# Optimization experiments

Measured on AMD Instinct MI355X. Metric: run time of the kernel, lower is better.

Reference implementation:

```python
import jax, jax.numpy as jnp
import numpy as np

HIDDEN = 4096
RANK = 4
DELTA = 1.0
BATCH = 4096


def glorot(key, shape):
    return jax.random.uniform(key, shape, minval=-1.0, maxval=1.0) * jnp.sqrt(2.0 / sum(shape))


def setup_inputs() -> dict:
    key = jax.random.key(0)
    k1, k2, k3, k4, k5, k6 = jax.random.split(key, 6)
    return {
        "h": jax.random.normal(k5, (BATCH, HIDDEN), dtype=jnp.float32),
        "x": jax.random.normal(k6, (BATCH, HIDDEN), dtype=jnp.float32),
        "a_diag": glorot(k1, (HIDDEN,)),
        "p_vec": glorot(k2, (HIDDEN, RANK)),
        "q_vec": glorot(k3, (HIDDEN, RANK)),
        "b_mat": glorot(k4, (HIDDEN, HIDDEN)),
    }


def reference(h, x, a_diag, p_vec, q_vec, b_mat):
    # Per-sample original math: (I + delta*(diag(a) + p q^T)) @ h + delta * b_mat.T @ x
    # Batched (rows of h/x are samples) with the Woodbury-style low-rank form:
    #   A_disc @ h  ->  h + delta*(a*h + (h @ q) @ p^T)
    #   B_disc^T @ x -> delta * (x @ b_mat)
    Ah = h + DELTA * (h * a_diag + (h @ q_vec) @ p_vec.T)  # [B, N]
    Bx = DELTA * (x @ b_mat)                               # [B, N]
    return Ah + Bx
```

## Files before the change

kernel.cpp:

```cpp
#include <hip/hip_runtime.h>
#include <hip/hip_bf16.h>
#include <stdint.h>
#include <stddef.h>

#define HIDDEN 4096
#define BATCH  4096
#define RANK   4

typedef _Float16 f16;
typedef __attribute__((ext_vector_type(8))) _Float16 half8;
typedef __attribute__((ext_vector_type(4))) float f32x4;
typedef __attribute__((ext_vector_type(8))) unsigned short ushort8;

#define ASYNC_COPY16(g, l)                                                     \
  __builtin_amdgcn_global_load_lds(                                            \
      (__attribute__((address_space(1))) void*)(g),                            \
      (__attribute__((address_space(3))) void*)(l), 16, 0, 0)

__global__ void cast_f16_kernel(const float* __restrict__ src, f16* __restrict__ dst) {
  size_t i = ((size_t)blockIdx.x * blockDim.x + threadIdx.x) * 8;
  float4 v0 = *(const float4*)(src + i);
  float4 v1 = *(const float4*)(src + i + 4);
  union { f16 h[8]; ushort8 v; } u;
  u.h[0] = (f16)v0.x; u.h[1] = (f16)v0.y; u.h[2] = (f16)v0.z; u.h[3] = (f16)v0.w;
  u.h[4] = (f16)v1.x; u.h[5] = (f16)v1.y; u.h[6] = (f16)v1.z; u.h[7] = (f16)v1.w;
  *(ushort8*)(dst + i) = u.v;
}

__global__ void transpose_cast_kernel(const float* __restrict__ B, f16* __restrict__ Bt) {
  __shared__ __align__(16) f16 tile[64 * 64];
  const int t = threadIdx.x;
  const int bx = blockIdx.x;
  const int by = blockIdx.y;
  const int tx = t & 15, ty = t >> 4;
  #pragma unroll
  for (int i = 0; i < 4; i++) {
    const int k = ty + i * 16;
    float4 v = *(const float4*)(B + (size_t)(by * 64 + k) * HIDDEN + bx * 64 + tx * 4);
    f16 hv[4];
    hv[0] = (f16)v.x; hv[1] = (f16)v.y; hv[2] = (f16)v.z; hv[3] = (f16)v.w;
    #pragma unroll
    for (int c = 0; c < 4; c++) {
      const int n = tx * 4 + c;
      const int phys = (k >> 3) ^ ((n >> 2) & 7);
      tile[n * 64 + phys * 8 + (k & 7)] = hv[c];
    }
  }
  __syncthreads();
  const int wx = t & 7, wy = t >> 3;
  #pragma unroll
  for (int i = 0; i < 2; i++) {
    const int n = wy + i * 32;
    const int phys = wx ^ ((n >> 2) & 7);
    ushort8 v = *(ushort8*)&tile[n * 64 + phys * 8];
    *(ushort8*)(Bt + (size_t)(bx * 64 + n) * HIDDEN + by * 64 + wx * 8) = v;
  }
}

__global__ void hq_kernel(const float* __restrict__ h, const float* __restrict__ q,
                          float* __restrict__ hq) {
  const int b = blockIdx.x;
  const float* hrow = h + (size_t)b * HIDDEN;
  float a0 = 0.f, a1 = 0.f, a2 = 0.f, a3 = 0.f;
  for (int k = threadIdx.x; k < HIDDEN; k += 256) {
    float hv = hrow[k];
    float4 qv = *(const float4*)(q + (size_t)k * RANK);
    a0 += hv * qv.x; a1 += hv * qv.y; a2 += hv * qv.z; a3 += hv * qv.w;
  }
  #pragma unroll
  for (int off = 32; off; off >>= 1) {
    a0 += __shfl_down(a0, off, 64);
    a1 += __shfl_down(a1, off, 64);
    a2 += __shfl_down(a2, off, 64);
    a3 += __shfl_down(a3, off, 64);
  }
  __shared__ float red[4][4];
  const int wave = threadIdx.x >> 6, lane = threadIdx.x & 63;
  if (lane == 0) { red[wave][0] = a0; red[wave][1] = a1; red[wave][2] = a2; red[wave][3] = a3; }
  __syncthreads();
  if (threadIdx.x < 4) {
    float s = red[0][threadIdx.x] + red[1][threadIdx.x] + red[2][threadIdx.x] + red[3][threadIdx.x];
    hq[(size_t)b * RANK + threadIdx.x] = s;
  }
}

#define GBM 256
#define GBN 256
#define GBK 64

#define BARRIER()                                   \
  do {                                              \
    asm volatile("" ::: "memory");                  \
    __builtin_amdgcn_s_barrier();                   \
    asm volatile("" ::: "memory");                  \
  } while (0)

#define VMWAIT0() asm volatile("s_waitcnt vmcnt(0)" ::: "memory")

#define STAGE_TILE(SBUF)                                                     \
  do {                                                                       \
    char* ad_ = (char*)(&As[SBUF][0]) + wave * 1024;                         \
    char* bd_ = (char*)(&Bs[SBUF][0]) + wave * 1024;                         \
    ASYNC_COPY16(ag + (size_t)0 * 64 * HIDDEN, ad_ + 0 * 8192);              \
    ASYNC_COPY16(bg + (size_t)0 * 64 * HIDDEN, bd_ + 0 * 8192);              \
    ASYNC_COPY16(ag + (size_t)1 * 64 * HIDDEN, ad_ + 1 * 8192);              \
    ASYNC_COPY16(bg + (size_t)1 * 64 * HIDDEN, bd_ + 1 * 8192);              \
    ASYNC_COPY16(ag + (size_t)2 * 64 * HIDDEN, ad_ + 2 * 8192);              \
    ASYNC_COPY16(bg + (size_t)2 * 64 * HIDDEN, bd_ + 2 * 8192);              \
    ASYNC_COPY16(ag + (size_t)3 * 64 * HIDDEN, ad_ + 3 * 8192);              \
    ASYNC_COPY16(bg + (size_t)3 * 64 * HIDDEN, bd_ + 3 * 8192);              \
    ag += GBK; bg += GBK;                                                    \
  } while (0)

#define LDF(base, R16, SG) (*(const half8*)((base) + (R16) * (16 * GBK) + (SG)))

#define MFMA4(I, AF)                                                                    \
  acc[I][0] = __builtin_amdgcn_mfma_f32_16x16x32_f16(AF, bf0, acc[I][0], 0, 0, 0);      \
  acc[I][1] = __builtin_amdgcn_mfma_f32_16x16x32_f16(AF, bf1, acc[I][1], 0, 0, 0);      \
  acc[I][2] = __builtin_amdgcn_mfma_f32_16x16x32_f16(AF, bf2, acc[I][2], 0, 0, 0);      \
  acc[I][3] = __builtin_amdgcn_mfma_f32_16x16x32_f16(AF, bf3, acc[I][3], 0, 0, 0);

#define TILE(BUF, SBUF, DO_STAGE)                                            \
  {                                                                          \
    const f16* Ab_ = &As[BUF][0] + (wm * 128 + fm) * GBK;                    \
    const f16* Bb_ = &Bs[BUF][0] + (wn * 64 + fm) * GBK;                     \
    const int sg0_ = ((0 + q) ^ sw) * 8;                                     \
    const int sg1_ = ((4 + q) ^ sw) * 8;                                     \
    half8 a0, a1, a2, a3, bf0, bf1, bf2, bf3;                                \
                         \
    a0 = LDF(Ab_, 0, sg0_); a1 = LDF(Ab_, 1, sg0_);                          \
    a2 = LDF(Ab_, 2, sg0_); a3 = LDF(Ab_, 3, sg0_);                          \
    bf0 = LDF(Bb_, 0, sg0_); bf1 = LDF(Bb_, 1, sg0_);                        \
    bf2 = LDF(Bb_, 2, sg0_); bf3 = LDF(Bb_, 3, sg0_);                        \
    if (DO_STAGE) STAGE_TILE(SBUF);                                          \
    BARRIER();                                                               \
    __builtin_amdgcn_s_setprio(1);                                           \
    MFMA4(0, a0) MFMA4(1, a1) MFMA4(2, a2) MFMA4(3, a3)                      \
    __builtin_amdgcn_s_setprio(0);                                           \
    BARRIER();                                                               \
                              \
    a0 = LDF(Ab_, 4, sg0_); a1 = LDF(Ab_, 5, sg0_);                          \
    a2 = LDF(Ab_, 6, sg0_); a3 = LDF(Ab_, 7, sg0_);                          \
    BARRIER();                                                               \
    __builtin_amdgcn_s_setprio(1);                                           \
    MFMA4(4, a0) MFMA4(5, a1) MFMA4(6, a2) MFMA4(7, a3)                      \
    __builtin_amdgcn_s_setprio(0);                                           \
    BARRIER();                                                               \
                                            \
    a0 = LDF(Ab_, 0, sg1_); a1 = LDF(Ab_, 1, sg1_);                          \
    a2 = LDF(Ab_, 2, sg1_); a3 = LDF(Ab_, 3, sg1_);                          \
    bf0 = LDF(Bb_, 0, sg1_); bf1 = LDF(Bb_, 1, sg1_);                        \
    bf2 = LDF(Bb_, 2, sg1_); bf3 = LDF(Bb_, 3, sg1_);                        \
    BARRIER();                                                               \
    __builtin_amdgcn_s_setprio(1);                                           \
    MFMA4(0, a0) MFMA4(1, a1) MFMA4(2, a2) MFMA4(3, a3)                      \
    __builtin_amdgcn_s_setprio(0);                                           \
    BARRIER();                                                               \
         \
    a0 = LDF(Ab_, 4, sg1_); a1 = LDF(Ab_, 5, sg1_);                          \
    a2 = LDF(Ab_, 6, sg1_); a3 = LDF(Ab_, 7, sg1_);                          \
    BARRIER();                                                               \
    __builtin_amdgcn_s_setprio(1);                                           \
    MFMA4(4, a0) MFMA4(5, a1) MFMA4(6, a2) MFMA4(7, a3)                      \
    __builtin_amdgcn_s_setprio(0);                                           \
    VMWAIT0();                                                               \
    BARRIER();                                                               \
  }

__global__ __launch_bounds__(512, 2) void gemm_fused_kernel(
    const f16* __restrict__ Xb, const f16* __restrict__ Bt,
    const float* __restrict__ h, const float* __restrict__ a_diag,
    const float* __restrict__ p_vec, const float* __restrict__ hq,
    float* __restrict__ out) {
  __shared__ __align__(16) f16 As[2][GBM * GBK];
  __shared__ __align__(16) f16 Bs[2][GBN * GBK];
  const int tid = threadIdx.x;
  const int bm = blockIdx.x, bn = blockIdx.y;
  const int wave = tid >> 6, lane = tid & 63;
  const int wm = wave >> 2, wn = wave & 3;

  const int srow = tid >> 3;
  const int gseg = (tid & 7) ^ (srow & 7);
  const f16* ag = Xb + (size_t)(bm * GBM + srow) * HIDDEN + gseg * 8;
  const f16* bg = Bt + (size_t)(bn * GBN + srow) * HIDDEN + gseg * 8;

  f32x4 acc[8][4];
  #pragma unroll
  for (int i = 0; i < 8; i++)
    #pragma unroll
    for (int j = 0; j < 4; j++)
      acc[i][j] = (f32x4){0.f, 0.f, 0.f, 0.f};

  const int q = lane >> 4;
  const int fm = lane & 15;
  const int sw = fm & 7;

  STAGE_TILE(0);
  VMWAIT0();
  BARRIER();

  #pragma unroll 1
  for (int kt2 = 0; kt2 < 31; ++kt2) {
    TILE(0, 1, true)
    TILE(1, 0, true)
  }
  TILE(0, 1, true)
  TILE(1, 0, false)

  float ad[4];
  float4 pv[4];
  #pragma unroll
  for (int j = 0; j < 4; j++) {
    const int gn = bn * GBN + wn * 64 + j * 16 + fm;
    ad[j] = 1.0f + a_diag[gn];
    pv[j] = *(const float4*)(p_vec + (size_t)gn * RANK);
  }
  #pragma unroll
  for (int i = 0; i < 8; i++) {
    #pragma unroll
    for (int r = 0; r < 4; r++) {
      const size_t gb = (size_t)(bm * GBM + wm * 128 + i * 16 + q * 4 + r);
      const float4 hv = *(const float4*)(hq + gb * RANK);
      const size_t rowoff = gb * HIDDEN + bn * GBN + wn * 64 + fm;
      #pragma unroll
      for (int j = 0; j < 4; j++) {
        const size_t idx = rowoff + j * 16;
        const float hval = __builtin_nontemporal_load(&h[idx]);
        const float v = acc[i][j][r] + hval * ad[j] +
                        hv.x * pv[j].x + hv.y * pv[j].y + hv.z * pv[j].z + hv.w * pv[j].w;
        __builtin_nontemporal_store(v, &out[idx]);
      }
    }
  }
}

__global__ void gemm_f32_fallback_kernel(const float* __restrict__ x, const float* __restrict__ bmat,
                                         const float* __restrict__ h, const float* __restrict__ a_diag,
                                         const float* __restrict__ p_vec, const float* __restrict__ hq,
                                         float* __restrict__ out) {
  __shared__ float As[16][64];
  __shared__ float Bs[16][68];
  const int t = threadIdx.x;
  const int bx = blockIdx.x, by = blockIdx.y;
  const int tm = t & 15, tn = t >> 4;
  float acc[4][4] = {{0.f}};
  for (int k0 = 0; k0 < HIDDEN; k0 += 16) {
    #pragma unroll
    for (int l = 0; l < 4; l++) {
      int idx = t + l * 256;
      int r = idx >> 4, k = idx & 15;
      As[k][r] = x[(size_t)(by * 64 + r) * HIDDEN + k0 + k];
      int kb = idx >> 6, nb = idx & 63;
      Bs[kb][nb] = bmat[(size_t)(k0 + kb) * HIDDEN + bx * 64 + nb];
    }
    __syncthreads();
    #pragma unroll
    for (int k = 0; k < 16; k++) {
      float av[4], bv[4];
      #pragma unroll
      for (int ii = 0; ii < 4; ii++) av[ii] = As[k][tm * 4 + ii];
      #pragma unroll
      for (int jj = 0; jj < 4; jj++) bv[jj] = Bs[k][tn * 4 + jj];
      #pragma unroll
      for (int ii = 0; ii < 4; ii++)
        #pragma unroll
        for (int jj = 0; jj < 4; jj++)
          acc[ii][jj] += av[ii] * bv[jj];
    }
    __syncthreads();
  }
  #pragma unroll
  for (int jj = 0; jj < 4; jj++) {
    int gn = bx * 64 + tn * 4 + jj;
    float ad = 1.0f + a_diag[gn];
    float4 pv = *(const float4*)(p_vec + (size_t)gn * RANK);
    #pragma unroll
    for (int ii = 0; ii < 4; ii++) {
      size_t gb = (size_t)(by * 64 + tm * 4 + ii);
      float4 hv = *(const float4*)(hq + gb * RANK);
      size_t idx = gb * HIDDEN + gn;
      out[idx] = acc[ii][jj] + h[idx] * ad +
                 hv.x * pv.x + hv.y * pv.y + hv.z * pv.z + hv.w * pv.w;
    }
  }
}

extern "C" void kernel_launch(void* const* d_in, const int* in_sizes, int n_in,
                              void* d_out, int out_size, void* d_ws, size_t ws_size,
                              hipStream_t stream) {
  const float* h      = (const float*)d_in[0];
  const float* x      = (const float*)d_in[1];
  const float* a_diag = (const float*)d_in[2];
  const float* p_vec  = (const float*)d_in[3];
  const float* q_vec  = (const float*)d_in[4];
  const float* b_mat  = (const float*)d_in[5];
  float* out = (float*)d_out;

  const size_t nElem = (size_t)BATCH * HIDDEN;
  const size_t hq_bytes = (size_t)BATCH * RANK * sizeof(float);
  const size_t need = hq_bytes + 2 * nElem * sizeof(f16);

  float* hq = (float*)d_ws;
  hq_kernel<<<BATCH, 256, 0, stream>>>(h, q_vec, hq);

  if (ws_size >= need) {
    f16* Xb = (f16*)((char*)d_ws + hq_bytes);
    f16* Bt = Xb + nElem;
    cast_f16_kernel<<<nElem / 2048, 256, 0, stream>>>(x, Xb);
    transpose_cast_kernel<<<dim3(HIDDEN / 64, HIDDEN / 64), 256, 0, stream>>>(b_mat, Bt);
    gemm_fused_kernel<<<dim3(BATCH / GBM, HIDDEN / GBN), 512, 0, stream>>>(
        Xb, Bt, h, a_diag, p_vec, hq, out);
  } else {
    gemm_f32_fallback_kernel<<<dim3(HIDDEN / 64, BATCH / 64), 256, 0, stream>>>(
        x, b_mat, h, a_diag, p_vec, hq, out);
  }
}
```

Before: 370.3 us.

## Spread global-to-LDS tile staging across compute phases with partial vmcnt waits

Each tile's eight async global-to-LDS copies are now split into four groups: B rows 0-1, B rows 2-3, A chunks 0/2 and A chunks 1/3. Each group is issued in a different MFMA phase instead of all at once. The end-of-tile wait changes from vmcnt(0) to vmcnt(2), so the last A-chunk copies can still be in flight when the next tile starts. The first phase of that tile only reads A chunks 0/2, and a mid-tile vmcnt(2) ensures chunks 1/3 have landed before they are read. The aim is to spread memory issue across the loop and shorten the full drain at each tile boundary, at the cost of tighter wait-count reasoning that must stay exactly in sync with the issue order.

```diff
diff --git a/kernel.cpp b/kernel.cpp
--- a/kernel.cpp
+++ b/kernel.cpp
@@ -96,19 +96,32 @@
   } while (0)
 
 #define VMWAIT0() asm volatile("s_waitcnt vmcnt(0)" ::: "memory")
-
-#define STAGE_TILE(SBUF)                                                     \
+#define VMWAIT2() asm volatile("s_waitcnt vmcnt(2)" ::: "memory")
+#define VMNOP()   do { } while (0)
+
+#define STAGE_B01(SBUF)                                                      \
+  do {                                                                       \
+    char* bd_ = (char*)(&Bs[SBUF][0]) + wave * 1024;                         \
+    ASYNC_COPY16(bg + (size_t)0 * 64 * HIDDEN, bd_ + 0 * 8192);              \
+    ASYNC_COPY16(bg + (size_t)1 * 64 * HIDDEN, bd_ + 1 * 8192);              \
+  } while (0)
+#define STAGE_B23(SBUF)                                                      \
+  do {                                                                       \
+    char* bd_ = (char*)(&Bs[SBUF][0]) + wave * 1024;                         \
+    ASYNC_COPY16(bg + (size_t)2 * 64 * HIDDEN, bd_ + 2 * 8192);              \
+    ASYNC_COPY16(bg + (size_t)3 * 64 * HIDDEN, bd_ + 3 * 8192);              \
+  } while (0)
+#define STAGE_A02(SBUF)                                                      \
   do {                                                                       \
     char* ad_ = (char*)(&As[SBUF][0]) + wave * 1024;                         \
-    char* bd_ = (char*)(&Bs[SBUF][0]) + wave * 1024;                         \
     ASYNC_COPY16(ag + (size_t)0 * 64 * HIDDEN, ad_ + 0 * 8192);              \
-    ASYNC_COPY16(bg + (size_t)0 * 64 * HIDDEN, bd_ + 0 * 8192);              \
+    ASYNC_COPY16(ag + (size_t)2 * 64 * HIDDEN, ad_ + 2 * 8192);              \
+  } while (0)
+#define STAGE_A13(SBUF)                                                      \
+  do {                                                                       \
+    char* ad_ = (char*)(&As[SBUF][0]) + wave * 1024;                         \
     ASYNC_COPY16(ag + (size_t)1 * 64 * HIDDEN, ad_ + 1 * 8192);              \
-    ASYNC_COPY16(bg + (size_t)1 * 64 * HIDDEN, bd_ + 1 * 8192);              \
-    ASYNC_COPY16(ag + (size_t)2 * 64 * HIDDEN, ad_ + 2 * 8192);              \
-    ASYNC_COPY16(bg + (size_t)2 * 64 * HIDDEN, bd_ + 2 * 8192);              \
     ASYNC_COPY16(ag + (size_t)3 * 64 * HIDDEN, ad_ + 3 * 8192);              \
-    ASYNC_COPY16(bg + (size_t)3 * 64 * HIDDEN, bd_ + 3 * 8192);              \
     ag += GBK; bg += GBK;                                                    \
   } while (0)
 
@@ -120,27 +133,29 @@
   acc[I][2] = __builtin_amdgcn_mfma_f32_16x16x32_f16(AF, bf2, acc[I][2], 0, 0, 0);      \
   acc[I][3] = __builtin_amdgcn_mfma_f32_16x16x32_f16(AF, bf3, acc[I][3], 0, 0, 0);
 
-#define TILE(BUF, SBUF, DO_STAGE)                                            \
+#define TILE(BUF, SBUF, DO_STAGE, WAITP0, WAITEND)                           \
   {                                                                          \
     const f16* Ab_ = &As[BUF][0] + (wm * 128 + fm) * GBK;                    \
     const f16* Bb_ = &Bs[BUF][0] + (wn * 64 + fm) * GBK;                     \
     const int sg0_ = ((0 + q) ^ sw) * 8;                                     \
     const int sg1_ = ((4 + q) ^ sw) * 8;                                     \
     half8 a0, a1, a2, a3, bf0, bf1, bf2, bf3;                                \
-                         \
+                                            \
     a0 = LDF(Ab_, 0, sg0_); a1 = LDF(Ab_, 1, sg0_);                          \
     a2 = LDF(Ab_, 2, sg0_); a3 = LDF(Ab_, 3, sg0_);                          \
     bf0 = LDF(Bb_, 0, sg0_); bf1 = LDF(Bb_, 1, sg0_);                        \
     bf2 = LDF(Bb_, 2, sg0_); bf3 = LDF(Bb_, 3, sg0_);                        \
-    if (DO_STAGE) STAGE_TILE(SBUF);                                          \
+    if (DO_STAGE) STAGE_B01(SBUF);                                           \
     BARRIER();                                                               \
     __builtin_amdgcn_s_setprio(1);                                           \
     MFMA4(0, a0) MFMA4(1, a1) MFMA4(2, a2) MFMA4(3, a3)                      \
     __builtin_amdgcn_s_setprio(0);                                           \
-    BARRIER();                                                               \
-                              \
+    WAITP0;                                                                  \
+    BARRIER();                                                               \
+                   \
     a0 = LDF(Ab_, 4, sg0_); a1 = LDF(Ab_, 5, sg0_);                          \
     a2 = LDF(Ab_, 6, sg0_); a3 = LDF(Ab_, 7, sg0_);                          \
+    if (DO_STAGE) STAGE_B23(SBUF);                                           \
     BARRIER();                                                               \
     __builtin_amdgcn_s_setprio(1);                                           \
     MFMA4(4, a0) MFMA4(5, a1) MFMA4(6, a2) MFMA4(7, a3)                      \
@@ -151,19 +166,21 @@
     a2 = LDF(Ab_, 2, sg1_); a3 = LDF(Ab_, 3, sg1_);                          \
     bf0 = LDF(Bb_, 0, sg1_); bf1 = LDF(Bb_, 1, sg1_);                        \
     bf2 = LDF(Bb_, 2, sg1_); bf3 = LDF(Bb_, 3, sg1_);                        \
+    if (DO_STAGE) STAGE_A02(SBUF);                                           \
     BARRIER();                                                               \
     __builtin_amdgcn_s_setprio(1);                                           \
     MFMA4(0, a0) MFMA4(1, a1) MFMA4(2, a2) MFMA4(3, a3)                      \
     __builtin_amdgcn_s_setprio(0);                                           \
     BARRIER();                                                               \
-         \
+                                            \
     a0 = LDF(Ab_, 4, sg1_); a1 = LDF(Ab_, 5, sg1_);                          \
     a2 = LDF(Ab_, 6, sg1_); a3 = LDF(Ab_, 7, sg1_);                          \
+    if (DO_STAGE) STAGE_A13(SBUF);                                           \
     BARRIER();                                                               \
     __builtin_amdgcn_s_setprio(1);                                           \
     MFMA4(4, a0) MFMA4(5, a1) MFMA4(6, a2) MFMA4(7, a3)                      \
     __builtin_amdgcn_s_setprio(0);                                           \
-    VMWAIT0();                                                               \
+    WAITEND;                                                                 \
     BARRIER();                                                               \
   }
 
@@ -195,17 +212,17 @@
   const int fm = lane & 15;
   const int sw = fm & 7;
 
-  STAGE_TILE(0);
-  VMWAIT0();
+  STAGE_B01(0); STAGE_B23(0); STAGE_A02(0); STAGE_A13(0);
+  VMWAIT2();
   BARRIER();
 
   #pragma unroll 1
   for (int kt2 = 0; kt2 < 31; ++kt2) {
-    TILE(0, 1, true)
-    TILE(1, 0, true)
-  }
-  TILE(0, 1, true)
-  TILE(1, 0, false)
+    TILE(0, 1, 1, VMWAIT2(), VMWAIT2())
+    TILE(1, 0, 1, VMWAIT2(), VMWAIT2())
+  }
+  TILE(0, 1, 1, VMWAIT2(), VMWAIT2())
+  TILE(1, 0, 0, VMWAIT0(), VMNOP())
 
   float ad[4];
   float4 pv[4];
```

Measured after the change: 362.1 us. 2.2% less time.

## Collapse per-tile barriers and overlap LDS fragment loads with MFMA; remap block indices

Applied to the files above, without the earlier changes.

Restructures the GEMM inner tile so there is one barrier per K-tile instead of about eight. It double-registers the A and B fragments (aA/aB, bE/bO) so LDS reads for the next MFMA quad are issued while the current quad runs, with sched_barrier fences to keep that order. It also remaps the linear block index so each group of blocks with the same index mod 8 (likely landing on one XCD) shares a compact set of bm/bn tiles, which should improve L2 reuse. This raises register pressure and relies on the single barrier plus the trailing vmcnt wait to keep the double-buffered LDS correct.

```diff
diff --git a/kernel.cpp b/kernel.cpp
--- a/kernel.cpp
+++ b/kernel.cpp
@@ -96,75 +96,78 @@
   } while (0)
 
 #define VMWAIT0() asm volatile("s_waitcnt vmcnt(0)" ::: "memory")
-
-#define STAGE_TILE(SBUF)                                                     \
+#define SBAR() __builtin_amdgcn_sched_barrier(0)
+
+#define STAGE_ALL(SBUF)                                                      \
   do {                                                                       \
     char* ad_ = (char*)(&As[SBUF][0]) + wave * 1024;                         \
     char* bd_ = (char*)(&Bs[SBUF][0]) + wave * 1024;                         \
+    ASYNC_COPY16(bg + (size_t)0 * 64 * HIDDEN, bd_ + 0 * 8192);              \
+    ASYNC_COPY16(bg + (size_t)1 * 64 * HIDDEN, bd_ + 1 * 8192);              \
+    ASYNC_COPY16(bg + (size_t)2 * 64 * HIDDEN, bd_ + 2 * 8192);              \
+    ASYNC_COPY16(bg + (size_t)3 * 64 * HIDDEN, bd_ + 3 * 8192);              \
     ASYNC_COPY16(ag + (size_t)0 * 64 * HIDDEN, ad_ + 0 * 8192);              \
-    ASYNC_COPY16(bg + (size_t)0 * 64 * HIDDEN, bd_ + 0 * 8192);              \
     ASYNC_COPY16(ag + (size_t)1 * 64 * HIDDEN, ad_ + 1 * 8192);              \
-    ASYNC_COPY16(bg + (size_t)1 * 64 * HIDDEN, bd_ + 1 * 8192);              \
     ASYNC_COPY16(ag + (size_t)2 * 64 * HIDDEN, ad_ + 2 * 8192);              \
-    ASYNC_COPY16(bg + (size_t)2 * 64 * HIDDEN, bd_ + 2 * 8192);              \
     ASYNC_COPY16(ag + (size_t)3 * 64 * HIDDEN, ad_ + 3 * 8192);              \
-    ASYNC_COPY16(bg + (size_t)3 * 64 * HIDDEN, bd_ + 3 * 8192);              \
     ag += GBK; bg += GBK;                                                    \
   } while (0)
 
 #define LDF(base, R16, SG) (*(const half8*)((base) + (R16) * (16 * GBK) + (SG)))
 
-#define MFMA4(I, AF)                                                                    \
-  acc[I][0] = __builtin_amdgcn_mfma_f32_16x16x32_f16(AF, bf0, acc[I][0], 0, 0, 0);      \
-  acc[I][1] = __builtin_amdgcn_mfma_f32_16x16x32_f16(AF, bf1, acc[I][1], 0, 0, 0);      \
-  acc[I][2] = __builtin_amdgcn_mfma_f32_16x16x32_f16(AF, bf2, acc[I][2], 0, 0, 0);      \
-  acc[I][3] = __builtin_amdgcn_mfma_f32_16x16x32_f16(AF, bf3, acc[I][3], 0, 0, 0);
+#define MQUAD(I0, AF, BF)                                                               \
+  __builtin_amdgcn_s_setprio(1);                                                        \
+  acc[I0+0][0] = __builtin_amdgcn_mfma_f32_16x16x32_f16(AF[0], BF[0], acc[I0+0][0], 0, 0, 0); \
+  acc[I0+0][1] = __builtin_amdgcn_mfma_f32_16x16x32_f16(AF[0], BF[1], acc[I0+0][1], 0, 0, 0); \
+  acc[I0+0][2] = __builtin_amdgcn_mfma_f32_16x16x32_f16(AF[0], BF[2], acc[I0+0][2], 0, 0, 0); \
+  acc[I0+0][3] = __builtin_amdgcn_mfma_f32_16x16x32_f16(AF[0], BF[3], acc[I0+0][3], 0, 0, 0); \
+  acc[I0+1][0] = __builtin_amdgcn_mfma_f32_16x16x32_f16(AF[1], BF[0], acc[I0+1][0], 0, 0, 0); \
+  acc[I0+1][1] = __builtin_amdgcn_mfma_f32_16x16x32_f16(AF[1], BF[1], acc[I0+1][1], 0, 0, 0); \
+  acc[I0+1][2] = __builtin_amdgcn_mfma_f32_16x16x32_f16(AF[1], BF[2], acc[I0+1][2], 0, 0, 0); \
+  acc[I0+1][3] = __builtin_amdgcn_mfma_f32_16x16x32_f16(AF[1], BF[3], acc[I0+1][3], 0, 0, 0); \
+  acc[I0+2][0] = __builtin_amdgcn_mfma_f32_16x16x32_f16(AF[2], BF[0], acc[I0+2][0], 0, 0, 0); \
+  acc[I0+2][1] = __builtin_amdgcn_mfma_f32_16x16x32_f16(AF[2], BF[1], acc[I0+2][1], 0, 0, 0); \
+  acc[I0+2][2] = __builtin_amdgcn_mfma_f32_16x16x32_f16(AF[2], BF[2], acc[I0+2][2], 0, 0, 0); \
+  acc[I0+2][3] = __builtin_amdgcn_mfma_f32_16x16x32_f16(AF[2], BF[3], acc[I0+2][3], 0, 0, 0); \
+  acc[I0+3][0] = __builtin_amdgcn_mfma_f32_16x16x32_f16(AF[3], BF[0], acc[I0+3][0], 0, 0, 0); \
+  acc[I0+3][1] = __builtin_amdgcn_mfma_f32_16x16x32_f16(AF[3], BF[1], acc[I0+3][1], 0, 0, 0); \
+  acc[I0+3][2] = __builtin_amdgcn_mfma_f32_16x16x32_f16(AF[3], BF[2], acc[I0+3][2], 0, 0, 0); \
+  acc[I0+3][3] = __builtin_amdgcn_mfma_f32_16x16x32_f16(AF[3], BF[3], acc[I0+3][3], 0, 0, 0); \
+  __builtin_amdgcn_s_setprio(0);
 
 #define TILE(BUF, SBUF, DO_STAGE)                                            \
   {                                                                          \
     const f16* Ab_ = &As[BUF][0] + (wm * 128 + fm) * GBK;                    \
     const f16* Bb_ = &Bs[BUF][0] + (wn * 64 + fm) * GBK;                     \
-    const int sg0_ = ((0 + q) ^ sw) * 8;                                     \
+    const int sg0_ = (q ^ sw) * 8;                                           \
     const int sg1_ = ((4 + q) ^ sw) * 8;                                     \
-    half8 a0, a1, a2, a3, bf0, bf1, bf2, bf3;                                \
-                         \
-    a0 = LDF(Ab_, 0, sg0_); a1 = LDF(Ab_, 1, sg0_);                          \
-    a2 = LDF(Ab_, 2, sg0_); a3 = LDF(Ab_, 3, sg0_);                          \
-    bf0 = LDF(Bb_, 0, sg0_); bf1 = LDF(Bb_, 1, sg0_);                        \
-    bf2 = LDF(Bb_, 2, sg0_); bf3 = LDF(Bb_, 3, sg0_);                        \
-    if (DO_STAGE) STAGE_TILE(SBUF);                                          \
+    half8 aA[4], aB[4], bE[4], bO[4];                                        \
     BARRIER();                                                               \
-    __builtin_amdgcn_s_setprio(1);                                           \
-    MFMA4(0, a0) MFMA4(1, a1) MFMA4(2, a2) MFMA4(3, a3)                      \
-    __builtin_amdgcn_s_setprio(0);                                           \
-    BARRIER();                                                               \
-                              \
-    a0 = LDF(Ab_, 4, sg0_); a1 = LDF(Ab_, 5, sg0_);                          \
-    a2 = LDF(Ab_, 6, sg0_); a3 = LDF(Ab_, 7, sg0_);                          \
-    BARRIER();                                                               \
-    __builtin_amdgcn_s_setprio(1);                                           \
-    MFMA4(4, a0) MFMA4(5, a1) MFMA4(6, a2) MFMA4(7, a3)                      \
-    __builtin_amdgcn_s_setprio(0);                                           \
-    BARRIER();                                                               \
-                                            \
-    a0 = LDF(Ab_, 0, sg1_); a1 = LDF(Ab_, 1, sg1_);                          \
-    a2 = LDF(Ab_, 2, sg1_); a3 = LDF(Ab_, 3, sg1_);                          \
-    bf0 = LDF(Bb_, 0, sg1_); bf1 = LDF(Bb_, 1, sg1_);                        \
-    bf2 = LDF(Bb_, 2, sg1_); bf3 = LDF(Bb_, 3, sg1_);                        \
-    BARRIER();                                                               \
-    __builtin_amdgcn_s_setprio(1);                                           \
-    MFMA4(0, a0) MFMA4(1, a1) MFMA4(2, a2) MFMA4(3, a3)                      \
-    __builtin_amdgcn_s_setprio(0);                                           \
-    BARRIER();                                                               \
-         \
-    a0 = LDF(Ab_, 4, sg1_); a1 = LDF(Ab_, 5, sg1_);                          \
-    a2 = LDF(Ab_, 6, sg1_); a3 = LDF(Ab_, 7, sg1_);                          \
-    BARRIER();                                                               \
-    __builtin_amdgcn_s_setprio(1);                                           \
-    MFMA4(4, a0) MFMA4(5, a1) MFMA4(6, a2) MFMA4(7, a3)                      \
-    __builtin_amdgcn_s_setprio(0);                                           \
-    VMWAIT0();                                                               \
-    BARRIER();                                                               \
+                                                    \
+    aA[0] = LDF(Ab_, 0, sg0_); aA[1] = LDF(Ab_, 1, sg0_);                    \
+    aA[2] = LDF(Ab_, 2, sg0_); aA[3] = LDF(Ab_, 3, sg0_);                    \
+    bE[0] = LDF(Bb_, 0, sg0_); bE[1] = LDF(Bb_, 1, sg0_);                    \
+    bE[2] = LDF(Bb_, 2, sg0_); bE[3] = LDF(Bb_, 3, sg0_);                    \
+    if (DO_STAGE) STAGE_ALL(SBUF);                                           \
+                                                  \
+    aB[0] = LDF(Ab_, 4, sg0_); aB[1] = LDF(Ab_, 5, sg0_);                    \
+    aB[2] = LDF(Ab_, 6, sg0_); aB[3] = LDF(Ab_, 7, sg0_);                    \
+    SBAR();                                                                  \
+    MQUAD(0, aA, bE)               \
+                        \
+    aA[0] = LDF(Ab_, 0, sg1_); aA[1] = LDF(Ab_, 1, sg1_);                    \
+    aA[2] = LDF(Ab_, 2, sg1_); aA[3] = LDF(Ab_, 3, sg1_);                    \
+    bO[0] = LDF(Bb_, 0, sg1_); bO[1] = LDF(Bb_, 1, sg1_);                    \
+    bO[2] = LDF(Bb_, 2, sg1_); bO[3] = LDF(Bb_, 3, sg1_);                    \
+    SBAR();                                                                  \
+    MQUAD(4, aB, bE)                                         \
+                                                  \
+    aB[0] = LDF(Ab_, 4, sg1_); aB[1] = LDF(Ab_, 5, sg1_);                    \
+    aB[2] = LDF(Ab_, 6, sg1_); aB[3] = LDF(Ab_, 7, sg1_);                    \
+    SBAR();                                                                  \
+    MQUAD(0, aA, bO)                                         \
+    MQUAD(4, aB, bO)                                         \
+    if (DO_STAGE) { VMWAIT0(); }                                             \
   }
 
 __global__ __launch_bounds__(512, 2) void gemm_fused_kernel(
@@ -175,7 +178,10 @@
   __shared__ __align__(16) f16 As[2][GBM * GBK];
   __shared__ __align__(16) f16 Bs[2][GBN * GBK];
   const int tid = threadIdx.x;
-  const int bm = blockIdx.x, bn = blockIdx.y;
+  const int lin = blockIdx.x + (blockIdx.y << 4);
+  const int xk = lin & 7, xr = lin >> 3;
+  const int bm = ((xk & 3) << 2) | (xr & 3);
+  const int bn = ((xk >> 2) << 3) | (xr >> 2);
   const int wave = tid >> 6, lane = tid & 63;
   const int wm = wave >> 2, wn = wave & 3;
 
@@ -195,17 +201,16 @@
   const int fm = lane & 15;
   const int sw = fm & 7;
 
-  STAGE_TILE(0);
+  STAGE_ALL(0);
   VMWAIT0();
-  BARRIER();
 
   #pragma unroll 1
   for (int kt2 = 0; kt2 < 31; ++kt2) {
-    TILE(0, 1, true)
-    TILE(1, 0, true)
-  }
-  TILE(0, 1, true)
-  TILE(1, 0, false)
+    TILE(0, 1, 1)
+    TILE(1, 0, 1)
+  }
+  TILE(0, 1, 1)
+  TILE(1, 0, 0)
 
   float ad[4];
   float4 pv[4];
```

Result: faster. 358.4 us (-3.2%).
